# Optimization experiments

Hardware: AMD Instinct MI355X
Metric: run time of the kernel (lower is better)

The kernel has to match this reference:

```python
import jax, jax.numpy as jnp
import numpy as np

EPS = 1e-12  # torch F.normalize eps


def _l2_normalize(x, axis=-1):
    n = jnp.linalg.norm(x, axis=axis, keepdims=True)
    return x / jnp.maximum(n, EPS)


def setup_inputs() -> dict:
    key = jax.random.key(0)
    k1, k2, k3 = jax.random.split(key, 3)
    B, T, IN_DIM = 8, 2000, 320
    NUM_BOOKS, CB_SIZE, CB_DIM = 1, 8192, 16
    hidden_states = jax.random.normal(k1, (B, T, IN_DIM), dtype=jnp.float32)
    # xavier_uniform_ on [num_books, in_dim, cb_dim]: fan_in=in_dim... torch impl uses
    # size(1)=in_dim as fan_in-ish and size(0)=num_books as fan_out with receptive=cb_dim
    fan_in = IN_DIM * CB_DIM
    fan_out = NUM_BOOKS * CB_DIM
    amp = np.sqrt(3.0) * np.sqrt(2.0 / (fan_in + fan_out))
    P = jax.random.uniform(k2, (NUM_BOOKS, IN_DIM, CB_DIM), dtype=jnp.float32,
                           minval=-amp, maxval=amp)
    CB = _l2_normalize(jax.random.normal(k3, (NUM_BOOKS, CB_SIZE, CB_DIM), dtype=jnp.float32))
    return {"hidden_states": hidden_states, "P": P, "CB": CB}


def reference(hidden_states, P, CB):
    # project: [B,T,D] x [N,D,E] -> [B,N,T,E], then L2-normalize last dim
    h = jnp.einsum('btd,nde->bnte', hidden_states, P)
    h = _l2_normalize(h)
    # Both h and CB rows are unit norm, so ||c - h||^2 = 2 - 2 c.h and
    # argmin_k ||CB[n,k] - h|| == argmax_k <CB[n,k], h>. This avoids the
    # [B,N,K,T,E] broadcast the torch code materializes.
    scores = jnp.einsum('bnte,nke->bntk', h, CB)  # [B,N,T,K]
    return jnp.argmax(scores, axis=-1)  # [B,N,T] int labels
```

## Files before the change

### kernel.cpp

```cpp
#include <hip/hip_runtime.h>
#include <stdint.h>

#define M_ROWS   16000
#define N_RT_PAD 1008
#define D_IN     320
#define E_DIM    16
#define K_CB     8192
#define NCHUNK   32
#define KT_PER_CHUNK 16
#define RPT      4
#define NRB      63

typedef __attribute__((ext_vector_type(8))) short bf16x8;
typedef __attribute__((ext_vector_type(4))) float f32x4;

#define XA_OFF   0u
#define XB_OFF   1032192u
#define CBA_OFF  2064384u
#define CBC_OFF  2588672u
#define PART_OFF 3112960u

#define AS1 __attribute__((address_space(1)))
#define AS3 __attribute__((address_space(3)))

__device__ __forceinline__ unsigned short f2bf(float x) {
    union { float f; unsigned u; } v; v.f = x;
    unsigned r = v.u + 0x7FFFu + ((v.u >> 16) & 1u);
    return (unsigned short)(r >> 16);
}
__device__ __forceinline__ float bf2f(unsigned short b) {
    union { unsigned u; float f; } v; v.u = ((unsigned)b) << 16; return v.f;
}

__global__ __launch_bounds__(256) void prep_kernel(const float* __restrict__ hs,
                                                   const float* __restrict__ P,
                                                   const float* __restrict__ CB,
                                                   unsigned short* __restrict__ Xa,
                                                   unsigned short* __restrict__ Xb,
                                                   unsigned short* __restrict__ CBa,
                                                   unsigned short* __restrict__ CBc) {
    int bid = blockIdx.x;
    int t   = threadIdx.x;
    if (bid < 250) {
        int row = bid * 64 + (t >> 2);
        int eq  = t & 3;
        if (row >= M_ROWS) return;
        const float* hrow = hs + (size_t)row * D_IN;
        float ax = 0.f, ay = 0.f, az = 0.f, aw = 0.f;
        #pragma unroll 4
        for (int d = 0; d < D_IN; d += 4) {
            float4 h4 = *reinterpret_cast<const float4*>(hrow + d);
            float4 p0 = *reinterpret_cast<const float4*>(P + (size_t)(d + 0) * E_DIM + eq * 4);
            float4 p1 = *reinterpret_cast<const float4*>(P + (size_t)(d + 1) * E_DIM + eq * 4);
            float4 p2 = *reinterpret_cast<const float4*>(P + (size_t)(d + 2) * E_DIM + eq * 4);
            float4 p3 = *reinterpret_cast<const float4*>(P + (size_t)(d + 3) * E_DIM + eq * 4);
            ax += h4.x * p0.x + h4.y * p1.x + h4.z * p2.x + h4.w * p3.x;
            ay += h4.x * p0.y + h4.y * p1.y + h4.z * p2.y + h4.w * p3.y;
            az += h4.x * p0.z + h4.y * p1.z + h4.z * p2.z + h4.w * p3.z;
            aw += h4.x * p0.w + h4.y * p1.w + h4.z * p2.w + h4.w * p3.w;
        }
        float v[4] = {ax, ay, az, aw};
        ushort4 h, m, l;
        unsigned short* hp = (unsigned short*)&h;
        unsigned short* mp = (unsigned short*)&m;
        unsigned short* lp = (unsigned short*)&l;
        #pragma unroll
        for (int i = 0; i < 4; ++i) {
            unsigned short hb = f2bf(v[i]);      float r1 = v[i] - bf2f(hb);
            unsigned short mb = f2bf(r1);        float r2 = r1 - bf2f(mb);
            unsigned short lb = f2bf(r2);
            hp[i] = hb; mp[i] = mb; lp[i] = lb;
        }
        int rt = row >> 4, rl = row & 15;
        int g  = eq >> 1;
        int j0 = (eq & 1) * 4;
        size_t base = (size_t)rt * 512;
        *reinterpret_cast<ushort4*>(Xa + base + ((g    ) * 16 + rl) * 8 + j0) = h;
        *reinterpret_cast<ushort4*>(Xa + base + ((2 + g) * 16 + rl) * 8 + j0) = m;
        *reinterpret_cast<ushort4*>(Xb + base + ((g    ) * 16 + rl) * 8 + j0) = l;
        *reinterpret_cast<ushort4*>(Xb + base + ((2 + g) * 16 + rl) * 8 + j0) = h;
    } else {
        int bid2 = bid - 250;
        int c  = bid2 * 64 + (t >> 2);
        int eq = t & 3;
        float4 v4 = *reinterpret_cast<const float4*>(CB + (size_t)c * E_DIM + eq * 4);
        float v[4] = {v4.x, v4.y, v4.z, v4.w};
        ushort4 h, m, l;
        unsigned short* hp = (unsigned short*)&h;
        unsigned short* mp = (unsigned short*)&m;
        unsigned short* lp = (unsigned short*)&l;
        #pragma unroll
        for (int i = 0; i < 4; ++i) {
            unsigned short hb = f2bf(v[i]);      float r1 = v[i] - bf2f(hb);
            unsigned short mb = f2bf(r1);        float r2 = r1 - bf2f(mb);
            unsigned short lb = f2bf(r2);
            hp[i] = hb; mp[i] = mb; lp[i] = lb;
        }
        int kt = c >> 4, cl = c & 15;
        int g  = eq >> 1;
        int j0 = (eq & 1) * 4;
        size_t base = (size_t)kt * 512;
        *reinterpret_cast<ushort4*>(CBa + base + ((g    ) * 16 + cl) * 8 + j0) = h;
        *reinterpret_cast<ushort4*>(CBa + base + ((2 + g) * 16 + cl) * 8 + j0) = m;
        *reinterpret_cast<ushort4*>(CBc + base + ((g    ) * 16 + cl) * 8 + j0) = h;
        *reinterpret_cast<ushort4*>(CBc + base + ((2 + g) * 16 + cl) * 8 + j0) = l;
    }
}

__global__ __launch_bounds__(256, 4) void score_kernel(const unsigned short* __restrict__ Xa,
                                                       const unsigned short* __restrict__ Xb,
                                                       const unsigned short* __restrict__ CBa,
                                                       const unsigned short* __restrict__ CBc,
                                                       unsigned long long* __restrict__ part) {
    __shared__ unsigned short sA[KT_PER_CHUNK * 512];
    __shared__ unsigned short sC[KT_PER_CHUNK * 512];

    int t    = threadIdx.x;
    int lane = t & 63;
    int w    = t >> 6;
    int flat = blockIdx.x;
    int xcd  = flat & 7;
    int idx  = flat >> 3;
    int kc   = xcd * 4 + idx / NRB;
    int rb   = idx % NRB;
    int rt0  = rb * 16 + w * RPT;

    bf16x8 a_hm[RPT], a_lh[RPT];
    #pragma unroll
    for (int r = 0; r < RPT; ++r) {
        a_hm[r] = *reinterpret_cast<const bf16x8*>(Xa + ((size_t)(rt0 + r) * 64 + lane) * 8);
        a_lh[r] = *reinterpret_cast<const bf16x8*>(Xb + ((size_t)(rt0 + r) * 64 + lane) * 8);
    }

    {
        const unsigned char* ga = (const unsigned char*)(CBa + (size_t)kc * KT_PER_CHUNK * 512);
        const unsigned char* gc = (const unsigned char*)(CBc + (size_t)kc * KT_PER_CHUNK * 512);
        unsigned char* la = (unsigned char*)sA;
        unsigned char* lc = (unsigned char*)sC;
        int wo = w * 1024 + lane * 16;
        #pragma unroll
        for (int q = 0; q < 4; ++q)
            __builtin_amdgcn_global_load_lds((const AS1 void*)(ga + q * 4096 + wo),
                                             (AS3 void*)(la + q * 4096 + w * 1024), 16, 0, 0);
        #pragma unroll
        for (int q = 0; q < 4; ++q)
            __builtin_amdgcn_global_load_lds((const AS1 void*)(gc + q * 4096 + wo),
                                             (AS3 void*)(lc + q * 4096 + w * 1024), 16, 0, 0);
    }

    float best[RPT][4];
    int   bidx[RPT][4];
    #pragma unroll
    for (int r = 0; r < RPT; ++r)
        #pragma unroll
        for (int i = 0; i < 4; ++i) { best[r][i] = -3.0e38f; bidx[r][i] = 0; }

    __syncthreads();

    const bf16x8* sA8 = reinterpret_cast<const bf16x8*>(sA);
    const bf16x8* sC8 = reinterpret_cast<const bf16x8*>(sC);
    int lsw = lane ^ 32;

    #pragma unroll 2
    for (int kt = 0; kt < KT_PER_CHUNK; ++kt) {
        bf16x8 c1 = sA8[kt * 64 + lane];
        bf16x8 c2 = sA8[kt * 64 + lsw];
        bf16x8 c3 = sC8[kt * 64 + lane];
        #pragma unroll
        for (int r = 0; r < RPT; ++r) {
            f32x4 acc = {0.f, 0.f, 0.f, 0.f};
            acc = __builtin_amdgcn_mfma_f32_16x16x32_bf16(a_hm[r], c1, acc, 0, 0, 0);
            acc = __builtin_amdgcn_mfma_f32_16x16x32_bf16(a_hm[r], c2, acc, 0, 0, 0);
            acc = __builtin_amdgcn_mfma_f32_16x16x32_bf16(a_lh[r], c3, acc, 0, 0, 0);
            #pragma unroll
            for (int i = 0; i < 4; ++i) {
                bool gt = acc[i] > best[r][i];
                best[r][i] = gt ? acc[i] : best[r][i];
                bidx[r][i] = gt ? kt     : bidx[r][i];
            }
        }
    }

    int colc = lane & 15;
    #pragma unroll
    for (int r = 0; r < RPT; ++r) {
        #pragma unroll
        for (int i = 0; i < 4; ++i) {
            unsigned u    = __float_as_uint(best[r][i]);
            unsigned mono = (u & 0x80000000u) ? ~u : (u | 0x80000000u);
            unsigned kg   = (unsigned)(kc * 256 + bidx[r][i] * 16 + colc);
            unsigned long long key = ((unsigned long long)mono << 32) | (unsigned)(~kg);
            #pragma unroll
            for (int off = 1; off <= 8; off <<= 1) {
                unsigned long long ok =
                    (((unsigned long long)(unsigned)__shfl_xor((int)(key >> 32), off, 64)) << 32) |
                    (unsigned)__shfl_xor((int)(unsigned)key, off, 64);
                key = (ok > key) ? ok : key;
            }
            if (colc == 0) {
                int row = (rt0 + r) * 16 + (lane >> 4) * 4 + i;
                if (row < M_ROWS) part[(size_t)row * NCHUNK + kc] = key;
            }
        }
    }
}

__global__ __launch_bounds__(256) void decode_kernel(const unsigned long long* __restrict__ part,
                                                     int* __restrict__ out) {
    int t    = threadIdx.x;
    int lane = t & 63;
    int wv   = t >> 6;
    int row  = blockIdx.x * 32 + wv * 8 + (lane >> 3);
    int j    = lane & 7;
    const unsigned long long* p = part + (size_t)row * NCHUNK + j * 4;
    unsigned long long k0 = p[0], k1 = p[1], k2 = p[2], k3 = p[3];
    k0 = k0 > k1 ? k0 : k1;
    k2 = k2 > k3 ? k2 : k3;
    unsigned long long key = k0 > k2 ? k0 : k2;
    #pragma unroll
    for (int off = 1; off <= 4; off <<= 1) {
        unsigned long long ok =
            (((unsigned long long)(unsigned)__shfl_xor((int)(key >> 32), off, 64)) << 32) |
            (unsigned)__shfl_xor((int)(unsigned)key, off, 64);
        key = (ok > key) ? ok : key;
    }
    if (j == 0) out[row] = (int)(~(unsigned)(key & 0xFFFFFFFFull));
}

extern "C" void kernel_launch(void* const* d_in, const int* in_sizes, int n_in,
                              void* d_out, int out_size, void* d_ws, size_t ws_size,
                              hipStream_t stream) {
    const float* hs = (const float*)d_in[0];
    const float* P  = (const float*)d_in[1];
    const float* CB = (const float*)d_in[2];
    int* out = (int*)d_out;

    char* ws = (char*)d_ws;
    unsigned short* Xa  = (unsigned short*)(ws + XA_OFF);
    unsigned short* Xb  = (unsigned short*)(ws + XB_OFF);
    unsigned short* CBa = (unsigned short*)(ws + CBA_OFF);
    unsigned short* CBc = (unsigned short*)(ws + CBC_OFF);
    unsigned long long* part = (unsigned long long*)(ws + PART_OFF);

    prep_kernel<<<dim3(378), dim3(256), 0, stream>>>(hs, P, CB, Xa, Xb, CBa, CBc);
    score_kernel<<<dim3(NRB * NCHUNK), dim3(256), 0, stream>>>(Xa, Xb, CBa, CBc, part);
    decode_kernel<<<dim3(M_ROWS / 32), dim3(256), 0, stream>>>(part, out);
}
```

Before: 57.59 us.

## Use single bf16x2 MFMA screening with exact fp32 rescoring of candidate chunks

Replaces the three-MFMA split-bf16 scoring (about fp32-exact) with one MFMA using hi/mid bf16 pairs, keeping only a per-chunk max score. A new argmax kernel rescans in exact fp32 only the codebook chunks whose approximate max lies within an error margin (0.012·||x||) of the global max. This cuts MFMA work, LDS traffic and per-element index tracking in the main loop. It raises score-kernel occupancy, but adds a data-dependent fp32 rescoring pass and relies on the error margin to keep results correct.

```diff
diff --git a/kernel.cpp b/kernel.cpp
--- a/kernel.cpp
+++ b/kernel.cpp
@@ -2,7 +2,6 @@
 #include <stdint.h>
 
 #define M_ROWS   16000
-#define N_RT_PAD 1008
 #define D_IN     320
 #define E_DIM    16
 #define K_CB     8192
@@ -15,10 +14,10 @@
 typedef __attribute__((ext_vector_type(4))) float f32x4;
 
 #define XA_OFF   0u
-#define XB_OFF   1032192u
-#define CBA_OFF  2064384u
-#define CBC_OFF  2588672u
-#define PART_OFF 3112960u
+#define CBA_OFF  1032192u
+#define XF_OFF   1556480u
+#define MG_OFF   2605056u
+#define PF_OFF   2670592u
 
 #define AS1 __attribute__((address_space(1)))
 #define AS3 __attribute__((address_space(3)))
@@ -36,9 +35,9 @@
                                                    const float* __restrict__ P,
                                                    const float* __restrict__ CB,
                                                    unsigned short* __restrict__ Xa,
-                                                   unsigned short* __restrict__ Xb,
-                                                   unsigned short* __restrict__ CBa,
-                                                   unsigned short* __restrict__ CBc) {
+                                                   float* __restrict__ Xf,
+                                                   float* __restrict__ Mg,
+                                                   unsigned short* __restrict__ CBa) {
     int bid = blockIdx.x;
     int t   = threadIdx.x;
     if (bid < 250) {
@@ -59,17 +58,21 @@
             az += h4.x * p0.z + h4.y * p1.z + h4.z * p2.z + h4.w * p3.z;
             aw += h4.x * p0.w + h4.y * p1.w + h4.z * p2.w + h4.w * p3.w;
         }
+        *reinterpret_cast<float4*>(Xf + (size_t)row * E_DIM + eq * 4) =
+            make_float4(ax, ay, az, aw);
+        float loc = ax * ax + ay * ay + az * az + aw * aw;
+        loc += __shfl_xor(loc, 1, 64);
+        loc += __shfl_xor(loc, 2, 64);
+        if (eq == 0) Mg[row] = 0.012f * sqrtf(loc);
         float v[4] = {ax, ay, az, aw};
-        ushort4 h, m, l;
+        ushort4 h, m;
         unsigned short* hp = (unsigned short*)&h;
         unsigned short* mp = (unsigned short*)&m;
-        unsigned short* lp = (unsigned short*)&l;
         #pragma unroll
         for (int i = 0; i < 4; ++i) {
-            unsigned short hb = f2bf(v[i]);      float r1 = v[i] - bf2f(hb);
-            unsigned short mb = f2bf(r1);        float r2 = r1 - bf2f(mb);
-            unsigned short lb = f2bf(r2);
-            hp[i] = hb; mp[i] = mb; lp[i] = lb;
+            unsigned short hb = f2bf(v[i]);
+            unsigned short mb = f2bf(v[i] - bf2f(hb));
+            hp[i] = hb; mp[i] = mb;
         }
         int rt = row >> 4, rl = row & 15;
         int g  = eq >> 1;
@@ -77,24 +80,20 @@
         size_t base = (size_t)rt * 512;
         *reinterpret_cast<ushort4*>(Xa + base + ((g    ) * 16 + rl) * 8 + j0) = h;
         *reinterpret_cast<ushort4*>(Xa + base + ((2 + g) * 16 + rl) * 8 + j0) = m;
-        *reinterpret_cast<ushort4*>(Xb + base + ((g    ) * 16 + rl) * 8 + j0) = l;
-        *reinterpret_cast<ushort4*>(Xb + base + ((2 + g) * 16 + rl) * 8 + j0) = h;
     } else {
         int bid2 = bid - 250;
         int c  = bid2 * 64 + (t >> 2);
         int eq = t & 3;
         float4 v4 = *reinterpret_cast<const float4*>(CB + (size_t)c * E_DIM + eq * 4);
         float v[4] = {v4.x, v4.y, v4.z, v4.w};
-        ushort4 h, m, l;
+        ushort4 h, m;
         unsigned short* hp = (unsigned short*)&h;
         unsigned short* mp = (unsigned short*)&m;
-        unsigned short* lp = (unsigned short*)&l;
         #pragma unroll
         for (int i = 0; i < 4; ++i) {
-            unsigned short hb = f2bf(v[i]);      float r1 = v[i] - bf2f(hb);
-            unsigned short mb = f2bf(r1);        float r2 = r1 - bf2f(mb);
-            unsigned short lb = f2bf(r2);
-            hp[i] = hb; mp[i] = mb; lp[i] = lb;
+            unsigned short hb = f2bf(v[i]);
+            unsigned short mb = f2bf(v[i] - bf2f(hb));
+            hp[i] = hb; mp[i] = mb;
         }
         int kt = c >> 4, cl = c & 15;
         int g  = eq >> 1;
@@ -102,18 +101,13 @@
         size_t base = (size_t)kt * 512;
         *reinterpret_cast<ushort4*>(CBa + base + ((g    ) * 16 + cl) * 8 + j0) = h;
         *reinterpret_cast<ushort4*>(CBa + base + ((2 + g) * 16 + cl) * 8 + j0) = m;
-        *reinterpret_cast<ushort4*>(CBc + base + ((g    ) * 16 + cl) * 8 + j0) = h;
-        *reinterpret_cast<ushort4*>(CBc + base + ((2 + g) * 16 + cl) * 8 + j0) = l;
-    }
-}
-
-__global__ __launch_bounds__(256, 4) void score_kernel(const unsigned short* __restrict__ Xa,
-                                                       const unsigned short* __restrict__ Xb,
+    }
+}
+
+__global__ __launch_bounds__(256, 8) void score_kernel(const unsigned short* __restrict__ Xa,
                                                        const unsigned short* __restrict__ CBa,
-                                                       const unsigned short* __restrict__ CBc,
-                                                       unsigned long long* __restrict__ part) {
+                                                       float* __restrict__ pf) {
     __shared__ unsigned short sA[KT_PER_CHUNK * 512];
-    __shared__ unsigned short sC[KT_PER_CHUNK * 512];
 
     int t    = threadIdx.x;
     int lane = t & 63;
@@ -125,106 +119,110 @@
     int rb   = idx % NRB;
     int rt0  = rb * 16 + w * RPT;
 
-    bf16x8 a_hm[RPT], a_lh[RPT];
-    #pragma unroll
-    for (int r = 0; r < RPT; ++r) {
+    bf16x8 a_hm[RPT];
+    #pragma unroll
+    for (int r = 0; r < RPT; ++r)
         a_hm[r] = *reinterpret_cast<const bf16x8*>(Xa + ((size_t)(rt0 + r) * 64 + lane) * 8);
-        a_lh[r] = *reinterpret_cast<const bf16x8*>(Xb + ((size_t)(rt0 + r) * 64 + lane) * 8);
-    }
 
     {
         const unsigned char* ga = (const unsigned char*)(CBa + (size_t)kc * KT_PER_CHUNK * 512);
-        const unsigned char* gc = (const unsigned char*)(CBc + (size_t)kc * KT_PER_CHUNK * 512);
         unsigned char* la = (unsigned char*)sA;
-        unsigned char* lc = (unsigned char*)sC;
         int wo = w * 1024 + lane * 16;
         #pragma unroll
         for (int q = 0; q < 4; ++q)
             __builtin_amdgcn_global_load_lds((const AS1 void*)(ga + q * 4096 + wo),
                                              (AS3 void*)(la + q * 4096 + w * 1024), 16, 0, 0);
-        #pragma unroll
-        for (int q = 0; q < 4; ++q)
-            __builtin_amdgcn_global_load_lds((const AS1 void*)(gc + q * 4096 + wo),
-                                             (AS3 void*)(lc + q * 4096 + w * 1024), 16, 0, 0);
     }
 
     float best[RPT][4];
-    int   bidx[RPT][4];
     #pragma unroll
     for (int r = 0; r < RPT; ++r)
         #pragma unroll
-        for (int i = 0; i < 4; ++i) { best[r][i] = -3.0e38f; bidx[r][i] = 0; }
+        for (int i = 0; i < 4; ++i) best[r][i] = -3.0e38f;
 
     __syncthreads();
 
     const bf16x8* sA8 = reinterpret_cast<const bf16x8*>(sA);
-    const bf16x8* sC8 = reinterpret_cast<const bf16x8*>(sC);
-    int lsw = lane ^ 32;
 
     #pragma unroll 2
     for (int kt = 0; kt < KT_PER_CHUNK; ++kt) {
         bf16x8 c1 = sA8[kt * 64 + lane];
-        bf16x8 c2 = sA8[kt * 64 + lsw];
-        bf16x8 c3 = sC8[kt * 64 + lane];
         #pragma unroll
         for (int r = 0; r < RPT; ++r) {
             f32x4 acc = {0.f, 0.f, 0.f, 0.f};
             acc = __builtin_amdgcn_mfma_f32_16x16x32_bf16(a_hm[r], c1, acc, 0, 0, 0);
-            acc = __builtin_amdgcn_mfma_f32_16x16x32_bf16(a_hm[r], c2, acc, 0, 0, 0);
-            acc = __builtin_amdgcn_mfma_f32_16x16x32_bf16(a_lh[r], c3, acc, 0, 0, 0);
             #pragma unroll
-            for (int i = 0; i < 4; ++i) {
-                bool gt = acc[i] > best[r][i];
-                best[r][i] = gt ? acc[i] : best[r][i];
-                bidx[r][i] = gt ? kt     : bidx[r][i];
+            for (int i = 0; i < 4; ++i) best[r][i] = fmaxf(best[r][i], acc[i]);
+        }
+    }
+
+    #pragma unroll
+    for (int r = 0; r < RPT; ++r) {
+        #pragma unroll
+        for (int i = 0; i < 4; ++i) {
+            float s = best[r][i];
+            #pragma unroll
+            for (int off = 1; off <= 8; off <<= 1)
+                s = fmaxf(s, __shfl_xor(s, off, 64));
+            if ((lane & 15) == 0) {
+                int row = (rt0 + r) * 16 + (lane >> 4) * 4 + i;
+                if (row < M_ROWS) pf[(size_t)row * NCHUNK + kc] = s;
             }
         }
     }
-
-    int colc = lane & 15;
-    #pragma unroll
-    for (int r = 0; r < RPT; ++r) {
-        #pragma unroll
-        for (int i = 0; i < 4; ++i) {
-            unsigned u    = __float_as_uint(best[r][i]);
-            unsigned mono = (u & 0x80000000u) ? ~u : (u | 0x80000000u);
-            unsigned kg   = (unsigned)(kc * 256 + bidx[r][i] * 16 + colc);
-            unsigned long long key = ((unsigned long long)mono << 32) | (unsigned)(~kg);
-            #pragma unroll
-            for (int off = 1; off <= 8; off <<= 1) {
-                unsigned long long ok =
-                    (((unsigned long long)(unsigned)__shfl_xor((int)(key >> 32), off, 64)) << 32) |
-                    (unsigned)__shfl_xor((int)(unsigned)key, off, 64);
-                key = (ok > key) ? ok : key;
-            }
-            if (colc == 0) {
-                int row = (rt0 + r) * 16 + (lane >> 4) * 4 + i;
-                if (row < M_ROWS) part[(size_t)row * NCHUNK + kc] = key;
-            }
-        }
-    }
-}
-
-__global__ __launch_bounds__(256) void decode_kernel(const unsigned long long* __restrict__ part,
+}
+
+__global__ __launch_bounds__(256) void argmax_kernel(const float* __restrict__ pf,
+                                                     const float* __restrict__ Mg,
+                                                     const float* __restrict__ Xf,
+                                                     const float* __restrict__ CB,
                                                      int* __restrict__ out) {
     int t    = threadIdx.x;
     int lane = t & 63;
-    int wv   = t >> 6;
-    int row  = blockIdx.x * 32 + wv * 8 + (lane >> 3);
-    int j    = lane & 7;
-    const unsigned long long* p = part + (size_t)row * NCHUNK + j * 4;
-    unsigned long long k0 = p[0], k1 = p[1], k2 = p[2], k3 = p[3];
-    k0 = k0 > k1 ? k0 : k1;
-    k2 = k2 > k3 ? k2 : k3;
-    unsigned long long key = k0 > k2 ? k0 : k2;
-    #pragma unroll
-    for (int off = 1; off <= 4; off <<= 1) {
-        unsigned long long ok =
-            (((unsigned long long)(unsigned)__shfl_xor((int)(key >> 32), off, 64)) << 32) |
-            (unsigned)__shfl_xor((int)(unsigned)key, off, 64);
-        key = (ok > key) ? ok : key;
-    }
-    if (j == 0) out[row] = (int)(~(unsigned)(key & 0xFFFFFFFFull));
+    int w    = t >> 6;
+    int row  = blockIdx.x * 4 + w;
+
+    float pv = pf[(size_t)row * NCHUNK + (lane & 31)];
+    float gmax = pv;
+    #pragma unroll
+    for (int off = 1; off <= 16; off <<= 1)
+        gmax = fmaxf(gmax, __shfl_xor(gmax, off, 64));
+    float thr = gmax - Mg[row];
+
+    float4 x0 = *reinterpret_cast<const float4*>(Xf + (size_t)row * E_DIM + 0);
+    float4 x1 = *reinterpret_cast<const float4*>(Xf + (size_t)row * E_DIM + 4);
+    float4 x2 = *reinterpret_cast<const float4*>(Xf + (size_t)row * E_DIM + 8);
+    float4 x3 = *reinterpret_cast<const float4*>(Xf + (size_t)row * E_DIM + 12);
+
+    float bs   = -3.0e38f;
+    int   bidx = 0x7FFFFFFF;
+    for (int kc = 0; kc < NCHUNK; ++kc) {
+        float cm = __shfl(pv, kc, 64);
+        if (cm >= thr) {
+            #pragma unroll
+            for (int j = 0; j < 4; ++j) {
+                int cw = kc * 256 + j * 64 + lane;
+                const float4* cp = reinterpret_cast<const float4*>(CB + (size_t)cw * E_DIM);
+                float4 c0 = cp[0], c1 = cp[1], c2 = cp[2], c3 = cp[3];
+                float s = x0.x * c0.x + x0.y * c0.y + x0.z * c0.z + x0.w * c0.w
+                        + x1.x * c1.x + x1.y * c1.y + x1.z * c1.z + x1.w * c1.w
+                        + x2.x * c2.x + x2.y * c2.y + x2.z * c2.z + x2.w * c2.w
+                        + x3.x * c3.x + x3.y * c3.y + x3.z * c3.z + x3.w * c3.w;
+                bool take = (s > bs) || (s == bs && cw < bidx);
+                bs   = take ? s  : bs;
+                bidx = take ? cw : bidx;
+            }
+        }
+    }
+    #pragma unroll
+    for (int off = 1; off <= 32; off <<= 1) {
+        float os = __shfl_xor(bs, off, 64);
+        int   oi = __shfl_xor(bidx, off, 64);
+        bool take = (os > bs) || (os == bs && oi < bidx);
+        bs   = take ? os : bs;
+        bidx = take ? oi : bidx;
+    }
+    if (lane == 0) out[row] = bidx;
 }
 
 extern "C" void kernel_launch(void* const* d_in, const int* in_sizes, int n_in,
@@ -237,12 +235,12 @@
 
     char* ws = (char*)d_ws;
     unsigned short* Xa  = (unsigned short*)(ws + XA_OFF);
-    unsigned short* Xb  = (unsigned short*)(ws + XB_OFF);
     unsigned short* CBa = (unsigned short*)(ws + CBA_OFF);
-    unsigned short* CBc = (unsigned short*)(ws + CBC_OFF);
-    unsigned long long* part = (unsigned long long*)(ws + PART_OFF);
-
-    prep_kernel<<<dim3(378), dim3(256), 0, stream>>>(hs, P, CB, Xa, Xb, CBa, CBc);
-    score_kernel<<<dim3(NRB * NCHUNK), dim3(256), 0, stream>>>(Xa, Xb, CBa, CBc, part);
-    decode_kernel<<<dim3(M_ROWS / 32), dim3(256), 0, stream>>>(part, out);
-}
+    float* Xf = (float*)(ws + XF_OFF);
+    float* Mg = (float*)(ws + MG_OFF);
+    float* pf = (float*)(ws + PF_OFF);
+
+    prep_kernel<<<dim3(378), dim3(256), 0, stream>>>(hs, P, CB, Xa, Xf, Mg, CBa);
+    score_kernel<<<dim3(NRB * NCHUNK), dim3(256), 0, stream>>>(Xa, CBa, pf);
+    argmax_kernel<<<dim3(M_ROWS / 4), dim3(256), 0, stream>>>(pf, Mg, Xf, CB, out);
+}
```

Result: slower. 67.30 us (+16.9%).
